# Kernel optimization log

Measured on AMD Instinct MI355X. Metric: run time of the kernel, lower is better.

## Reference

```python
import jax, jax.numpy as jnp
import numpy as np

SIGMA = 0.1
B, C, H, W = 2, 3, 64, 64


def setup_inputs() -> dict:
    key = jax.random.key(0)
    x = jax.random.uniform(key, (B, C, H, W), dtype=jnp.float32)
    return {"x": x}


def reference(x) -> jnp.ndarray:
    """Range-only bilateral filter: out[p] = sum_q K(p,q) x[q] / sum_q K(p,q),
    K(p,q) = exp(-((x_q - x_p)/sigma)^2), all-pairs over the H*W pixels,
    independently per (batch, channel)."""
    b, c, h, w = x.shape
    n = h * w
    xf = x.reshape(b, c, n)                      # [B,C,N]
    # pairwise intensity differences -> Gaussian range kernel [B,C,N,N]
    diff = xf[:, :, :, None] - xf[:, :, None, :]
    K = jnp.exp(-jnp.square(diff / SIGMA))
    num = jnp.einsum('bcpq,bcq->bcp', K, xf)     # weighted sum over source pixels
    den = jnp.sum(K, axis=-1)                    # normalization
    return (num / den).reshape(b, c, h, w)
```

## Files before the change

### kernel.cpp

```cpp
#include <hip/hip_runtime.h>

#define NSLICE 6
#define NPIX   4096
#define M      20

#define C0         0.088622693f
#define TWO_C0     0.177245385f
#define AEXP_LOG2  0.035597112f
#define DEN0       362.99854f

__global__ __launch_bounds__(256) void moments_kernel(
        const float* __restrict__ x, float* __restrict__ ws) {
    const int mi = blockIdx.x;
    const int s  = blockIdx.y;
    const float fm = (float)(mi + 1);
    const int tid = threadIdx.x;
    const float4* x4 = (const float4*)(x + s * NPIX);

    float Sc = 0.f, Ss = 0.f, Tc = 0.f, Ts = 0.f, X = 0.f;
    #pragma unroll
    for (int j = 0; j < NPIX / 4 / 256; ++j) {
        float4 v4 = x4[j * 256 + tid];
        float vv[4] = {v4.x, v4.y, v4.z, v4.w};
        #pragma unroll
        for (int k = 0; k < 4; ++k) {
            float v   = vv[k];
            float arg = 0.5f * fm * v;
            float sn  = __builtin_amdgcn_sinf(arg);
            float cn  = __builtin_amdgcn_cosf(arg);
            Sc += cn;  Ss += sn;
            Tc = fmaf(v, cn, Tc);
            Ts = fmaf(v, sn, Ts);
            X += v;
        }
    }

    #pragma unroll
    for (int off = 1; off < 64; off <<= 1) {
        Sc += __shfl_xor(Sc, off);  Ss += __shfl_xor(Ss, off);
        Tc += __shfl_xor(Tc, off);  Ts += __shfl_xor(Ts, off);
        X  += __shfl_xor(X,  off);
    }
    __shared__ float red[4][5];
    const int w = tid >> 6;
    if ((tid & 63) == 0) {
        red[w][0] = Sc; red[w][1] = Ss; red[w][2] = Tc; red[w][3] = Ts; red[w][4] = X;
    }
    __syncthreads();
    if (tid == 0) {
        float sc = 0.f, ss = 0.f, tc = 0.f, ts = 0.f, xx = 0.f;
        #pragma unroll
        for (int ww = 0; ww < 4; ++ww) {
            sc += red[ww][0]; ss += red[ww][1]; tc += red[ww][2];
            ts += red[ww][3]; xx += red[ww][4];
        }
        float coef = TWO_C0 * __builtin_amdgcn_exp2f(-AEXP_LOG2 * fm * fm);
        float* f = ws + (s * (M + 1) + (mi + 1)) * 4;
        f[0] = coef * sc;  f[1] = coef * ss;
        f[2] = coef * tc;  f[3] = coef * ts;
        if (mi == 0) {
            float* f0 = ws + s * (M + 1) * 4;
            f0[0] = DEN0;  f0[1] = C0 * xx;  f0[2] = 0.f;  f0[3] = 0.f;
        }
    }
}

__global__ __launch_bounds__(512) void recombine_kernel(
        const float* __restrict__ x, const float* __restrict__ ws,
        float* __restrict__ out) {
    const int s = blockIdx.y;
    const int p = blockIdx.x * 512 + threadIdx.x;
    __shared__ __align__(16) float fin[(M + 1) * 4];
    if (threadIdx.x < (M + 1) * 4)
        fin[threadIdx.x] = ws[s * (M + 1) * 4 + threadIdx.x];
    __syncthreads();

    const float v  = x[s * NPIX + p];
    const float s1 = __builtin_amdgcn_sinf(0.5f * v);
    const float c1 = __builtin_amdgcn_cosf(0.5f * v);
    const float4* F = (const float4*)fin;

    float4 f0 = F[0], f1 = F[1];
    float den = f0.x, num = f0.y;
    den = fmaf(c1, f1.x, den);  den = fmaf(s1, f1.y, den);
    num = fmaf(c1, f1.z, num);  num = fmaf(s1, f1.w, num);

    const float tc = c1 + c1;
    float cm2 = 1.f, sm2 = 0.f, cm1 = c1, sm1 = s1;
    #pragma unroll
    for (int m = 2; m <= M; ++m) {
        float cn = fmaf(tc, cm1, -cm2);
        float sn = fmaf(tc, sm1, -sm2);
        cm2 = cm1; cm1 = cn; sm2 = sm1; sm1 = sn;
        float4 f = F[m];
        den = fmaf(cn, f.x, den);  den = fmaf(sn, f.y, den);
        num = fmaf(cn, f.z, num);  num = fmaf(sn, f.w, num);
    }
    out[s * NPIX + p] = num / den;
}

extern "C" void kernel_launch(void* const* d_in, const int* in_sizes, int n_in,
                              void* d_out, int out_size, void* d_ws, size_t ws_size,
                              hipStream_t stream) {
    const float* x = (const float*)d_in[0];
    float* out = (float*)d_out;
    float* ws  = (float*)d_ws;
    moments_kernel<<<dim3(M, NSLICE), dim3(256), 0, stream>>>(x, ws);
    recombine_kernel<<<dim3(NPIX / 512, NSLICE), dim3(512), 0, stream>>>(x, ws, out);
}
```

Before: 55.32 us.

## Fuse moments and recombine kernels into one block per slice

Replaces the two-kernel pipeline with a single kernel where one 1024-thread block per slice loads the slice into LDS, computes the Fourier moments across waves, and then evaluates the output per pixel with four pixels per thread. This removes the second launch and the global workspace round trip. In exchange, the moment computation now runs on only six blocks, so parallelism across the GPU is much lower and each wave serializes up to two moments.

New measurement: 60.07 us. +8.6%, slower.

```diff
diff --git a/kernel.cpp b/kernel.cpp
--- a/kernel.cpp
+++ b/kernel.cpp
@@ -3,108 +3,104 @@
 #define NSLICE 6
 #define NPIX   4096
 #define M      20
+#define NWAVE  16
 
 #define C0         0.088622693f
 #define TWO_C0     0.177245385f
 #define AEXP_LOG2  0.035597112f
 #define DEN0       362.99854f
 
-__global__ __launch_bounds__(256) void moments_kernel(
-        const float* __restrict__ x, float* __restrict__ ws) {
-    const int mi = blockIdx.x;
-    const int s  = blockIdx.y;
-    const float fm = (float)(mi + 1);
-    const int tid = threadIdx.x;
-    const float4* x4 = (const float4*)(x + s * NPIX);
+__global__ __launch_bounds__(1024) void bilateral_fused(
+        const float* __restrict__ x, float* __restrict__ out) {
+    const int s    = blockIdx.x;
+    const int tid  = threadIdx.x;
+    const int wid  = tid >> 6;
+    const int lane = tid & 63;
 
-    float Sc = 0.f, Ss = 0.f, Tc = 0.f, Ts = 0.f, X = 0.f;
+    __shared__ __align__(16) float xs[NPIX];
+    __shared__ __align__(16) float fin[(M + 1) * 4];
+    __shared__ float red[NWAVE];
+
+    const float4 v4 = ((const float4*)(x + s * NPIX))[tid];
+    ((float4*)xs)[tid] = v4;
+
+    float xsum = (v4.x + v4.y) + (v4.z + v4.w);
     #pragma unroll
-    for (int j = 0; j < NPIX / 4 / 256; ++j) {
-        float4 v4 = x4[j * 256 + tid];
-        float vv[4] = {v4.x, v4.y, v4.z, v4.w};
+    for (int off = 1; off < 64; off <<= 1) xsum += __shfl_xor(xsum, off);
+    if (lane == 0) red[wid] = xsum;
+    __syncthreads();
+
+    if (tid == 0) {
+        float X = 0.f;
         #pragma unroll
-        for (int k = 0; k < 4; ++k) {
-            float v   = vv[k];
-            float arg = 0.5f * fm * v;
-            float sn  = __builtin_amdgcn_sinf(arg);
-            float cn  = __builtin_amdgcn_cosf(arg);
-            Sc += cn;  Ss += sn;
-            Tc = fmaf(v, cn, Tc);
-            Ts = fmaf(v, sn, Ts);
-            X += v;
+        for (int w = 0; w < NWAVE; ++w) X += red[w];
+        fin[0] = DEN0; fin[1] = C0 * X; fin[2] = 0.f; fin[3] = 0.f;
+    }
+
+    for (int m = wid + 1; m <= M; m += NWAVE) {
+        const float fm = (float)m;
+        float Sc = 0.f, Ss = 0.f, Tc = 0.f, Ts = 0.f;
+        #pragma unroll 8
+        for (int i = 0; i < NPIX / 128; ++i) {
+            float p0 = xs[i * 128 + lane];
+            float p1 = xs[i * 128 + 64 + lane];
+            float a0 = 0.5f * fm * p0;
+            float a1 = 0.5f * fm * p1;
+            float sn0 = __builtin_amdgcn_sinf(a0), cn0 = __builtin_amdgcn_cosf(a0);
+            float sn1 = __builtin_amdgcn_sinf(a1), cn1 = __builtin_amdgcn_cosf(a1);
+            Sc += cn0 + cn1;  Ss += sn0 + sn1;
+            Tc = fmaf(p0, cn0, Tc);  Tc = fmaf(p1, cn1, Tc);
+            Ts = fmaf(p0, sn0, Ts);  Ts = fmaf(p1, sn1, Ts);
+        }
+        #pragma unroll
+        for (int off = 1; off < 64; off <<= 1) {
+            Sc += __shfl_xor(Sc, off);  Ss += __shfl_xor(Ss, off);
+            Tc += __shfl_xor(Tc, off);  Ts += __shfl_xor(Ts, off);
+        }
+        if (lane == 0) {
+            float coef = TWO_C0 * __builtin_amdgcn_exp2f(-AEXP_LOG2 * fm * fm);
+            float* f = fin + m * 4;
+            f[0] = coef * Sc;  f[1] = coef * Ss;
+            f[2] = coef * Tc;  f[3] = coef * Ts;
         }
     }
+    __syncthreads();
 
+    const float4* F = (const float4*)fin;
+    const float vv[4] = {v4.x, v4.y, v4.z, v4.w};
+    float c1[4], s1[4], t2[4], cm1[4], cm2[4], sm1[4], sm2[4], den[4], num[4];
+    const float4 f0 = F[0], f1 = F[1];
     #pragma unroll
-    for (int off = 1; off < 64; off <<= 1) {
-        Sc += __shfl_xor(Sc, off);  Ss += __shfl_xor(Ss, off);
-        Tc += __shfl_xor(Tc, off);  Ts += __shfl_xor(Ts, off);
-        X  += __shfl_xor(X,  off);
+    for (int j = 0; j < 4; ++j) {
+        s1[j] = __builtin_amdgcn_sinf(0.5f * vv[j]);
+        c1[j] = __builtin_amdgcn_cosf(0.5f * vv[j]);
+        den[j] = fmaf(c1[j], f1.x, f0.x);  den[j] = fmaf(s1[j], f1.y, den[j]);
+        num[j] = fmaf(c1[j], f1.z, f0.y);  num[j] = fmaf(s1[j], f1.w, num[j]);
+        t2[j]  = c1[j] + c1[j];
+        cm2[j] = 1.f;  sm2[j] = 0.f;  cm1[j] = c1[j];  sm1[j] = s1[j];
     }
-    __shared__ float red[4][5];
-    const int w = tid >> 6;
-    if ((tid & 63) == 0) {
-        red[w][0] = Sc; red[w][1] = Ss; red[w][2] = Tc; red[w][3] = Ts; red[w][4] = X;
-    }
-    __syncthreads();
-    if (tid == 0) {
-        float sc = 0.f, ss = 0.f, tc = 0.f, ts = 0.f, xx = 0.f;
+    #pragma unroll
+    for (int m2 = 2; m2 <= M; ++m2) {
+        const float4 f = F[m2];
         #pragma unroll
-        for (int ww = 0; ww < 4; ++ww) {
-            sc += red[ww][0]; ss += red[ww][1]; tc += red[ww][2];
-            ts += red[ww][3]; xx += red[ww][4];
-        }
-        float coef = TWO_C0 * __builtin_amdgcn_exp2f(-AEXP_LOG2 * fm * fm);
-        float* f = ws + (s * (M + 1) + (mi + 1)) * 4;
-        f[0] = coef * sc;  f[1] = coef * ss;
-        f[2] = coef * tc;  f[3] = coef * ts;
-        if (mi == 0) {
-            float* f0 = ws + s * (M + 1) * 4;
-            f0[0] = DEN0;  f0[1] = C0 * xx;  f0[2] = 0.f;  f0[3] = 0.f;
+        for (int j = 0; j < 4; ++j) {
+            float cn = fmaf(t2[j], cm1[j], -cm2[j]);
+            float sn = fmaf(t2[j], sm1[j], -sm2[j]);
+            cm2[j] = cm1[j];  cm1[j] = cn;  sm2[j] = sm1[j];  sm1[j] = sn;
+            den[j] = fmaf(cn, f.x, den[j]);  den[j] = fmaf(sn, f.y, den[j]);
+            num[j] = fmaf(cn, f.z, num[j]);  num[j] = fmaf(sn, f.w, num[j]);
         }
     }
-}
-
-__global__ __launch_bounds__(512) void recombine_kernel(
-        const float* __restrict__ x, const float* __restrict__ ws,
-        float* __restrict__ out) {
-    const int s = blockIdx.y;
-    const int p = blockIdx.x * 512 + threadIdx.x;
-    __shared__ __align__(16) float fin[(M + 1) * 4];
-    if (threadIdx.x < (M + 1) * 4)
-        fin[threadIdx.x] = ws[s * (M + 1) * 4 + threadIdx.x];
-    __syncthreads();
-
-    const float v  = x[s * NPIX + p];
-    const float s1 = __builtin_amdgcn_sinf(0.5f * v);
-    const float c1 = __builtin_amdgcn_cosf(0.5f * v);
-    const float4* F = (const float4*)fin;
-
-    float4 f0 = F[0], f1 = F[1];
-    float den = f0.x, num = f0.y;
-    den = fmaf(c1, f1.x, den);  den = fmaf(s1, f1.y, den);
-    num = fmaf(c1, f1.z, num);  num = fmaf(s1, f1.w, num);
-
-    const float tc = c1 + c1;
-    float cm2 = 1.f, sm2 = 0.f, cm1 = c1, sm1 = s1;
-    #pragma unroll
-    for (int m = 2; m <= M; ++m) {
-        float cn = fmaf(tc, cm1, -cm2);
-        float sn = fmaf(tc, sm1, -sm2);
-        cm2 = cm1; cm1 = cn; sm2 = sm1; sm1 = sn;
-        float4 f = F[m];
-        den = fmaf(cn, f.x, den);  den = fmaf(sn, f.y, den);
-        num = fmaf(cn, f.z, num);  num = fmaf(sn, f.w, num);
-    }
-    out[s * NPIX + p] = num / den;
+    float4 o;
+    o.x = num[0] / den[0];  o.y = num[1] / den[1];
+    o.z = num[2] / den[2];  o.w = num[3] / den[3];
+    ((float4*)(out + s * NPIX))[tid] = o;
 }
 
 extern "C" void kernel_launch(void* const* d_in, const int* in_sizes, int n_in,
                               void* d_out, int out_size, void* d_ws, size_t ws_size,
                               hipStream_t stream) {
-    const float* x = (const float*)d_in[0];
-    float* out = (float*)d_out;
-    float* ws  = (float*)d_ws;
-    moments_kernel<<<dim3(M, NSLICE), dim3(256), 0, stream>>>(x, ws);
-    recombine_kernel<<<dim3(NPIX / 512, NSLICE), dim3(512), 0, stream>>>(x, ws, out);
+    (void)in_sizes; (void)n_in; (void)out_size; (void)d_ws; (void)ws_size;
+    bilateral_fused<<<dim3(NSLICE), dim3(1024), 0, stream>>>(
+        (const float*)d_in[0], (float*)d_out);
 }
```
